# Kernel optimization log

Measured on AMD Instinct MI355X. Metric: run time of the kernel, lower is better.

The kernel has to match this reference:

```python
import jax, jax.numpy as jnp
import numpy as np

IN_DIM = 256
CODE_LEN = 128
MEM_LEN = 65536
BETA = 1.0


def setup_inputs() -> dict:
    key = jax.random.key(0)
    k1, k2, k3, k4, k5, k6 = jax.random.split(key, 6)
    x = jax.random.normal(k1, (1, IN_DIM), dtype=jnp.float32)
    memory = jax.random.normal(k2, (MEM_LEN, CODE_LEN), dtype=jnp.float32)
    mem_data = jax.random.normal(k3, (MEM_LEN, IN_DIM), dtype=jnp.float32)
    mem_idx = jnp.arange(MEM_LEN, dtype=jnp.int64) if jax.config.jax_enable_x64 else jnp.arange(MEM_LEN, dtype=jnp.int32)
    W = jax.random.normal(k4, (CODE_LEN, IN_DIM), dtype=jnp.float32) / np.sqrt(IN_DIM)
    b = jax.random.normal(k5, (CODE_LEN,), dtype=jnp.float32) * 0.01
    count = jnp.array(0, dtype=jnp.int32)
    return {"x": x, "memory": memory, "mem_data": mem_data, "mem_idx": mem_idx,
            "W": W, "b": b, "count": count}


def reference(x, memory, mem_data, mem_idx, W, b, count):
    # mean/std normalization using memory bank statistics (torch .std uses ddof=1)
    mean = mem_data.mean(axis=0)                      # [in_dim]
    std = mem_data.std(axis=0, ddof=1)                # [in_dim]
    new = (x - mean) / std
    new = jnp.where(std == 0, 0.0, new)               # [1, in_dim]
    # linear encode
    enc = new @ W.T + b                               # [1, code_len]
    # L1 distance to every memory slot, take min
    dists = jnp.sum(jnp.abs(memory - enc), axis=1)    # [mem_len]
    loss = dists.min()
    # conditional scatter update of memory / mem_data / mem_idx
    do_update = loss <= BETA
    pos = jnp.argmin(mem_idx)
    new_memory = jnp.where(do_update,
                           memory.at[pos].set(enc[0]), memory)
    new_mem_data = jnp.where(do_update,
                             mem_data.at[pos].set(x[0]), mem_data)
    new_mem_idx = jnp.where(do_update,
                            mem_idx.at[pos].set(count.astype(mem_idx.dtype)), mem_idx)
    return loss, new_memory, new_mem_data, new_mem_idx
```

## Files before the change

kernel.cpp:

```cpp
#include <hip/hip_runtime.h>
#include <hip/hip_bf16.h>

#define IN_DIM   256
#define CODE_LEN 128
#define MEM_LEN  65536
#define BETA     1.0f

#define OUT_MEM_OFF   1
#define OUT_MD_OFF    (1 + MEM_LEN*CODE_LEN)
#define OUT_IDX_OFF   (OUT_MD_OFF + MEM_LEN*IN_DIM)

#define WS_COLSUM 0
#define WS_COLSQ  256
#define WS_ENC    512
#define WS_LOSS   640
#define WS_KEY    642
#define WS_CTR2   644

#define MD_ELEMS  (MEM_LEN*IN_DIM)
#define MD_TILES  (MD_ELEMS/4)
#define MEM_ELEMS (MEM_LEN*CODE_LEN)
#define MEM_TILES (MEM_ELEMS/4)

typedef float vfloat4 __attribute__((ext_vector_type(4)));

__device__ __forceinline__ void store16u(float* dst, vfloat4 v) {
    __builtin_memcpy(dst, &v, 16);
}

__global__ void k_init(float* __restrict__ ws) {
    const int t = threadIdx.x;
    #pragma unroll
    for (int j = 0; j < 8; ++j) ws[t + j * 64] = 0.f;
    if (t == 0) {
        ((unsigned int*)ws)[WS_LOSS] = 0xFFFFFFFFu;
        *((unsigned long long*)(ws + WS_KEY)) = ~0ull;
        ((unsigned int*)ws)[WS_CTR2] = 0u;
    }
}

__global__ __launch_bounds__(256, 4) void k_stats_enc(
        const float* __restrict__ x,
        const float* __restrict__ mem_data,
        const int*   __restrict__ mem_idx,
        const float* __restrict__ W,
        const float* __restrict__ b,
        float* __restrict__ out,
        float* __restrict__ ws) {
    const int t = threadIdx.x;

    if (blockIdx.x >= 1024) {
        __shared__ unsigned long long red[256];
        const int tid = (blockIdx.x - 1024) * 256 + t;
        unsigned long long local = ~0ull;
        #pragma unroll
        for (int rep = 0; rep < 4; ++rep) {
            int i = tid + rep * 16384;
            int v = mem_idx[i];
            out[OUT_IDX_OFF + i] = (float)v;
            unsigned long long key =
                (((unsigned long long)(unsigned int)(v ^ (int)0x80000000)) << 32)
                | (unsigned int)i;
            local = local < key ? local : key;
        }
        red[t] = local;
        __syncthreads();
        for (int s = 128; s > 0; s >>= 1) {
            if (t < s) { unsigned long long o = red[t + s]; if (o < red[t]) red[t] = o; }
            __syncthreads();
        }
        if (t == 0) atomicMin((unsigned long long*)(ws + WS_KEY), red[0]);
    } else {
        __shared__ float lsum[256], lsq[256];
        float* __restrict__ out_md = out + OUT_MD_OFF;
        const int t0 = blockIdx.x * 256 + t;
        float s0=0,s1=0,s2=0,s3=0,q0=0,q1=0,q2=0,q3=0;

        vfloat4 v[16];
        #pragma unroll
        for (int j = 0; j < 16; ++j)
            v[j] = ((const vfloat4*)mem_data)[t0 + j * 262144];
        #pragma unroll
        for (int j = 0; j < 16; ++j) {
            const int k = t0 + j * 262144;
            store16u(out_md + 4 * k, v[j]);
            s0 += v[j].x; q0 += v[j].x * v[j].x;
            s1 += v[j].y; q1 += v[j].y * v[j].y;
            s2 += v[j].z; q2 += v[j].z * v[j].z;
            s3 += v[j].w; q3 += v[j].w * v[j].w;
        }

        lsum[t] = 0.f; lsq[t] = 0.f;
        __syncthreads();
        const int c0 = (4 * t) & 255;
        atomicAdd(&lsum[c0    ], s0);  atomicAdd(&lsq[c0    ], q0);
        atomicAdd(&lsum[c0 + 1], s1);  atomicAdd(&lsq[c0 + 1], q1);
        atomicAdd(&lsum[c0 + 2], s2);  atomicAdd(&lsq[c0 + 2], q2);
        atomicAdd(&lsum[c0 + 3], s3);  atomicAdd(&lsq[c0 + 3], q3);
        __syncthreads();
        atomicAdd(&ws[WS_COLSUM + t], lsum[t]);
        atomicAdd(&ws[WS_COLSQ  + t], lsq[t]);
    }

    asm volatile("s_waitcnt vmcnt(0)" ::: "memory");
    __syncthreads();
    __shared__ unsigned int s_last;
    if (t == 0)
        s_last = (atomicAdd(&((unsigned int*)ws)[WS_CTR2], 1u) == 1087u) ? 1u : 0u;
    __syncthreads();
    if (!s_last) return;

    __shared__ float nrm[IN_DIM];
    {
        float sum = atomicAdd(&ws[WS_COLSUM + t], 0.0f);
        float sq  = atomicAdd(&ws[WS_COLSQ  + t], 0.0f);
        float mean = sum * (1.0f / MEM_LEN);
        float var  = (sq - sum * sum * (1.0f / MEM_LEN)) * (1.0f / (MEM_LEN - 1));
        var = fmaxf(var, 0.0f);
        float sd = sqrtf(var);
        nrm[t] = (sd == 0.0f) ? 0.0f : (x[t] - mean) / sd;
    }
    __syncthreads();
    if (t < CODE_LEN) {
        float acc = b[t];
        const float* w = W + t * IN_DIM;
        #pragma unroll 8
        for (int d = 0; d < IN_DIM; ++d) acc += nrm[d] * w[d];
        ws[WS_ENC + t] = acc;
    }
}

__global__ __launch_bounds__(256, 4) void k_dist_copy(
        const float* __restrict__ memory,
        float* __restrict__ out,
        float* __restrict__ ws) {
    __shared__ vfloat4 es[32];
    __shared__ float red[256];
    const int t = threadIdx.x;
    if (t < 32) es[t] = ((const vfloat4*)(ws + WS_ENC))[t];
    __syncthreads();
    const int lane = t & 31;
    const int grp  = t >> 5;
    const vfloat4 e = es[lane];
    float* __restrict__ out_mem = out + OUT_MEM_OFF;
    float localmin = 3.4e38f;
    #pragma unroll
    for (int half = 0; half < 2; ++half) {
        vfloat4 m[4];
        int idx[4];
        #pragma unroll
        for (int sw = 0; sw < 4; ++sw) {
            const int row = (half * 4 + sw) * 8192 + blockIdx.x * 8 + grp;
            const int i = row * 32 + lane;
            idx[sw] = i;
            m[sw] = ((const vfloat4*)memory)[i];
        }
        #pragma unroll
        for (int sw = 0; sw < 4; ++sw) {
            const int i = idx[sw];
            store16u(out_mem + 4 * i, m[sw]);
            float d = fabsf(m[sw].x-e.x) + fabsf(m[sw].y-e.y)
                    + fabsf(m[sw].z-e.z) + fabsf(m[sw].w-e.w);
            #pragma unroll
            for (int off = 16; off > 0; off >>= 1) d += __shfl_xor(d, off, 32);
            localmin = fminf(localmin, d);
        }
    }
    red[t] = localmin;
    __syncthreads();
    for (int s2 = 128; s2 > 0; s2 >>= 1) {
        if (t < s2) red[t] = fminf(red[t], red[t + s2]);
        __syncthreads();
    }
    if (t == 0)
        atomicMin((unsigned int*)(ws + WS_LOSS), __float_as_uint(red[0]));
}

__global__ void k_final(const float* __restrict__ x,
                        const int* __restrict__ count,
                        const float* __restrict__ ws,
                        float* __restrict__ d_out) {
    const int t = threadIdx.x;
    const float loss = __uint_as_float(((const unsigned int*)ws)[WS_LOSS]);
    if (t == 0) d_out[0] = loss;
    if (loss <= BETA) {
        unsigned long long key = *(const unsigned long long*)(ws + WS_KEY);
        unsigned int pos = (unsigned int)(key & 0xFFFFFFFFull);
        if (t < CODE_LEN)
            d_out[OUT_MEM_OFF + (size_t)pos * CODE_LEN + t] = ws[WS_ENC + t];
        d_out[OUT_MD_OFF + (size_t)pos * IN_DIM + t] = x[t];
        if (t == 0)
            d_out[OUT_IDX_OFF + pos] = (float)count[0];
    }
}

extern "C" void kernel_launch(void* const* d_in, const int* in_sizes, int n_in,
                              void* d_out, int out_size, void* d_ws, size_t ws_size,
                              hipStream_t stream) {
    const float* x        = (const float*)d_in[0];
    const float* memory   = (const float*)d_in[1];
    const float* mem_data = (const float*)d_in[2];
    const int*   mem_idx  = (const int*)d_in[3];
    const float* W        = (const float*)d_in[4];
    const float* b        = (const float*)d_in[5];
    const int*   count    = (const int*)d_in[6];
    float* out = (float*)d_out;
    float* ws  = (float*)d_ws;

    k_init<<<1, 64, 0, stream>>>(ws);
    k_stats_enc<<<1088, 256, 0, stream>>>(x, mem_data, mem_idx, W, b, out, ws);
    k_dist_copy<<<1024, 256, 0, stream>>>(memory, out, ws);
    k_final<<<1, 256, 0, stream>>>(x, count, ws, out);
}
```

Before: 220.7 us.

## Split stats and encode kernels, widen grids, replicate atomic accumulators

Replaces the last-block-done counter with a separate single-block encode kernel. The column-stat atomics are spread over 16 replicated partial-sum slots, placed in the not-yet-written memory region of the output, and the loss atomicMin is spread over 8 slots. The stats and distance kernels now use 4x and 2x more blocks, each doing less work per thread, with a higher occupancy hint. The aim is less atomic contention, more memory-level parallelism and no serialized tail block, at the cost of one extra kernel launch and reuse of output memory as scratch.

```diff
diff --git a/kernel.cpp b/kernel.cpp
--- a/kernel.cpp
+++ b/kernel.cpp
@@ -1,5 +1,4 @@
 #include <hip/hip_runtime.h>
-#include <hip/hip_bf16.h>
 
 #define IN_DIM   256
 #define CODE_LEN 128
@@ -10,17 +9,15 @@
 #define OUT_MD_OFF    (1 + MEM_LEN*CODE_LEN)
 #define OUT_IDX_OFF   (OUT_MD_OFF + MEM_LEN*IN_DIM)
 
-#define WS_COLSUM 0
-#define WS_COLSQ  256
-#define WS_ENC    512
-#define WS_LOSS   640
-#define WS_KEY    642
-#define WS_CTR2   644
-
-#define MD_ELEMS  (MEM_LEN*IN_DIM)
-#define MD_TILES  (MD_ELEMS/4)
-#define MEM_ELEMS (MEM_LEN*CODE_LEN)
-#define MEM_TILES (MEM_ELEMS/4)
+#define WS_ENC   0
+#define WS_LOSS  128
+#define WS_KEY   136
+
+#define SB_OFF    OUT_MEM_OFF
+#define N_REP     16
+
+#define MD_TILES  (MEM_LEN*IN_DIM/4)
+#define MEM_TILES (MEM_LEN*CODE_LEN/4)
 
 typedef float vfloat4 __attribute__((ext_vector_type(4)));
 
@@ -28,30 +25,25 @@
     __builtin_memcpy(dst, &v, 16);
 }
 
-__global__ void k_init(float* __restrict__ ws) {
-    const int t = threadIdx.x;
-    #pragma unroll
-    for (int j = 0; j < 8; ++j) ws[t + j * 64] = 0.f;
-    if (t == 0) {
-        ((unsigned int*)ws)[WS_LOSS] = 0xFFFFFFFFu;
-        *((unsigned long long*)(ws + WS_KEY)) = ~0ull;
-        ((unsigned int*)ws)[WS_CTR2] = 0u;
-    }
-}
-
-__global__ __launch_bounds__(256, 4) void k_stats_enc(
-        const float* __restrict__ x,
+__global__ void k_init(float* __restrict__ out, float* __restrict__ ws) {
+    const int t = threadIdx.x;
+    #pragma unroll
+    for (int j = 0; j < 2 * N_REP; ++j) out[SB_OFF + t + j * 256] = 0.f;
+    if (t < 8) ((unsigned int*)ws)[WS_LOSS + t] = 0xFFFFFFFFu;
+    if (t == 0) *((unsigned long long*)(ws + WS_KEY)) = ~0ull;
+}
+
+__global__ __launch_bounds__(256, 8) void k_stats(
         const float* __restrict__ mem_data,
         const int*   __restrict__ mem_idx,
-        const float* __restrict__ W,
-        const float* __restrict__ b,
         float* __restrict__ out,
         float* __restrict__ ws) {
     const int t = threadIdx.x;
-
-    if (blockIdx.x >= 1024) {
+    const int bid = blockIdx.x;
+
+    if (bid >= 4096) {
         __shared__ unsigned long long red[256];
-        const int tid = (blockIdx.x - 1024) * 256 + t;
+        const int tid = (bid - 4096) * 256 + t;
         unsigned long long local = ~0ull;
         #pragma unroll
         for (int rep = 0; rep < 4; ++rep) {
@@ -70,56 +62,59 @@
             __syncthreads();
         }
         if (t == 0) atomicMin((unsigned long long*)(ws + WS_KEY), red[0]);
-    } else {
-        __shared__ float lsum[256], lsq[256];
-        float* __restrict__ out_md = out + OUT_MD_OFF;
-        const int t0 = blockIdx.x * 256 + t;
-        float s0=0,s1=0,s2=0,s3=0,q0=0,q1=0,q2=0,q3=0;
-
-        vfloat4 v[16];
-        #pragma unroll
-        for (int j = 0; j < 16; ++j)
-            v[j] = ((const vfloat4*)mem_data)[t0 + j * 262144];
-        #pragma unroll
-        for (int j = 0; j < 16; ++j) {
-            const int k = t0 + j * 262144;
-            store16u(out_md + 4 * k, v[j]);
-            s0 += v[j].x; q0 += v[j].x * v[j].x;
-            s1 += v[j].y; q1 += v[j].y * v[j].y;
-            s2 += v[j].z; q2 += v[j].z * v[j].z;
-            s3 += v[j].w; q3 += v[j].w * v[j].w;
-        }
-
-        lsum[t] = 0.f; lsq[t] = 0.f;
-        __syncthreads();
-        const int c0 = (4 * t) & 255;
-        atomicAdd(&lsum[c0    ], s0);  atomicAdd(&lsq[c0    ], q0);
-        atomicAdd(&lsum[c0 + 1], s1);  atomicAdd(&lsq[c0 + 1], q1);
-        atomicAdd(&lsum[c0 + 2], s2);  atomicAdd(&lsq[c0 + 2], q2);
-        atomicAdd(&lsum[c0 + 3], s3);  atomicAdd(&lsq[c0 + 3], q3);
-        __syncthreads();
-        atomicAdd(&ws[WS_COLSUM + t], lsum[t]);
-        atomicAdd(&ws[WS_COLSQ  + t], lsq[t]);
-    }
-
-    asm volatile("s_waitcnt vmcnt(0)" ::: "memory");
-    __syncthreads();
-    __shared__ unsigned int s_last;
-    if (t == 0)
-        s_last = (atomicAdd(&((unsigned int*)ws)[WS_CTR2], 1u) == 1087u) ? 1u : 0u;
-    __syncthreads();
-    if (!s_last) return;
-
+        return;
+    }
+
+    __shared__ float lsum[256], lsq[256];
+    lsum[t] = 0.f; lsq[t] = 0.f;
+    __syncthreads();
+
+    float* __restrict__ out_md = out + OUT_MD_OFF;
+    const int gtid = bid * 256 + t;
+    float s0=0,s1=0,s2=0,s3=0,q0=0,q1=0,q2=0,q3=0;
+
+    vfloat4 v[4];
+    #pragma unroll
+    for (int i = 0; i < 4; ++i)
+        v[i] = ((const vfloat4*)mem_data)[gtid + i * 1048576];
+    #pragma unroll
+    for (int i = 0; i < 4; ++i) {
+        store16u(out_md + 4 * (gtid + i * 1048576), v[i]);
+        s0 += v[i].x; q0 += v[i].x * v[i].x;
+        s1 += v[i].y; q1 += v[i].y * v[i].y;
+        s2 += v[i].z; q2 += v[i].z * v[i].z;
+        s3 += v[i].w; q3 += v[i].w * v[i].w;
+    }
+
+    const int c0 = (4 * t) & 255;
+    atomicAdd(&lsum[c0    ], s0);  atomicAdd(&lsq[c0    ], q0);
+    atomicAdd(&lsum[c0 + 1], s1);  atomicAdd(&lsq[c0 + 1], q1);
+    atomicAdd(&lsum[c0 + 2], s2);  atomicAdd(&lsq[c0 + 2], q2);
+    atomicAdd(&lsum[c0 + 3], s3);  atomicAdd(&lsq[c0 + 3], q3);
+    __syncthreads();
+    float* __restrict__ sb = out + SB_OFF + (bid & (N_REP - 1)) * 512;
+    atomicAdd(&sb[t      ], lsum[t]);
+    atomicAdd(&sb[t + 256], lsq[t]);
+}
+
+__global__ void k_enc(const float* __restrict__ x,
+                      const float* __restrict__ W,
+                      const float* __restrict__ b,
+                      const float* __restrict__ out,
+                      float* __restrict__ ws) {
     __shared__ float nrm[IN_DIM];
-    {
-        float sum = atomicAdd(&ws[WS_COLSUM + t], 0.0f);
-        float sq  = atomicAdd(&ws[WS_COLSQ  + t], 0.0f);
-        float mean = sum * (1.0f / MEM_LEN);
-        float var  = (sq - sum * sum * (1.0f / MEM_LEN)) * (1.0f / (MEM_LEN - 1));
-        var = fmaxf(var, 0.0f);
-        float sd = sqrtf(var);
-        nrm[t] = (sd == 0.0f) ? 0.0f : (x[t] - mean) / sd;
-    }
+    const int t = threadIdx.x;
+    float sum = 0.f, sq = 0.f;
+    #pragma unroll
+    for (int r = 0; r < N_REP; ++r) {
+        sum += out[SB_OFF + r * 512 + t];
+        sq  += out[SB_OFF + r * 512 + 256 + t];
+    }
+    float mean = sum * (1.0f / MEM_LEN);
+    float var  = (sq - sum * sum * (1.0f / MEM_LEN)) * (1.0f / (MEM_LEN - 1));
+    var = fmaxf(var, 0.0f);
+    float sd = sqrtf(var);
+    nrm[t] = (sd == 0.0f) ? 0.0f : (x[t] - mean) / sd;
     __syncthreads();
     if (t < CODE_LEN) {
         float acc = b[t];
@@ -130,7 +125,7 @@
     }
 }
 
-__global__ __launch_bounds__(256, 4) void k_dist_copy(
+__global__ __launch_bounds__(256, 8) void k_dist(
         const float* __restrict__ memory,
         float* __restrict__ out,
         float* __restrict__ ws) {
@@ -140,32 +135,25 @@
     if (t < 32) es[t] = ((const vfloat4*)(ws + WS_ENC))[t];
     __syncthreads();
     const int lane = t & 31;
-    const int grp  = t >> 5;
     const vfloat4 e = es[lane];
     float* __restrict__ out_mem = out + OUT_MEM_OFF;
+    const int gtid = blockIdx.x * 256 + t;
     float localmin = 3.4e38f;
-    #pragma unroll
-    for (int half = 0; half < 2; ++half) {
-        vfloat4 m[4];
-        int idx[4];
+
+    vfloat4 m[4];
+    #pragma unroll
+    for (int i = 0; i < 4; ++i)
+        m[i] = ((const vfloat4*)memory)[gtid + i * 524288];
+    #pragma unroll
+    for (int i = 0; i < 4; ++i) {
+        store16u(out_mem + 4 * (gtid + i * 524288), m[i]);
+        float d = fabsf(m[i].x - e.x) + fabsf(m[i].y - e.y)
+                + fabsf(m[i].z - e.z) + fabsf(m[i].w - e.w);
         #pragma unroll
-        for (int sw = 0; sw < 4; ++sw) {
-            const int row = (half * 4 + sw) * 8192 + blockIdx.x * 8 + grp;
-            const int i = row * 32 + lane;
-            idx[sw] = i;
-            m[sw] = ((const vfloat4*)memory)[i];
-        }
-        #pragma unroll
-        for (int sw = 0; sw < 4; ++sw) {
-            const int i = idx[sw];
-            store16u(out_mem + 4 * i, m[sw]);
-            float d = fabsf(m[sw].x-e.x) + fabsf(m[sw].y-e.y)
-                    + fabsf(m[sw].z-e.z) + fabsf(m[sw].w-e.w);
-            #pragma unroll
-            for (int off = 16; off > 0; off >>= 1) d += __shfl_xor(d, off, 32);
-            localmin = fminf(localmin, d);
-        }
-    }
+        for (int off = 16; off > 0; off >>= 1) d += __shfl_xor(d, off, 32);
+        localmin = fminf(localmin, d);
+    }
+
     red[t] = localmin;
     __syncthreads();
     for (int s2 = 128; s2 > 0; s2 >>= 1) {
@@ -173,7 +161,8 @@
         __syncthreads();
     }
     if (t == 0)
-        atomicMin((unsigned int*)(ws + WS_LOSS), __float_as_uint(red[0]));
+        atomicMin((unsigned int*)(ws + WS_LOSS + (blockIdx.x & 7)),
+                  __float_as_uint(red[0]));
 }
 
 __global__ void k_final(const float* __restrict__ x,
@@ -181,7 +170,13 @@
                         const float* __restrict__ ws,
                         float* __restrict__ d_out) {
     const int t = threadIdx.x;
-    const float loss = __uint_as_float(((const unsigned int*)ws)[WS_LOSS]);
+    unsigned int lb = ((const unsigned int*)ws)[WS_LOSS];
+    #pragma unroll
+    for (int r = 1; r < 8; ++r) {
+        unsigned int o = ((const unsigned int*)ws)[WS_LOSS + r];
+        lb = o < lb ? o : lb;
+    }
+    const float loss = __uint_as_float(lb);
     if (t == 0) d_out[0] = loss;
     if (loss <= BETA) {
         unsigned long long key = *(const unsigned long long*)(ws + WS_KEY);
@@ -207,8 +202,9 @@
     float* out = (float*)d_out;
     float* ws  = (float*)d_ws;
 
-    k_init<<<1, 64, 0, stream>>>(ws);
-    k_stats_enc<<<1088, 256, 0, stream>>>(x, mem_data, mem_idx, W, b, out, ws);
-    k_dist_copy<<<1024, 256, 0, stream>>>(memory, out, ws);
+    k_init<<<1, 256, 0, stream>>>(out, ws);
+    k_stats<<<4160, 256, 0, stream>>>(mem_data, mem_idx, out, ws);
+    k_enc<<<1, 256, 0, stream>>>(x, W, b, out, ws);
+    k_dist<<<2048, 256, 0, stream>>>(memory, out, ws);
     k_final<<<1, 256, 0, stream>>>(x, count, ws, out);
 }
```

Result: slower. 239.0 us (+8.3%).

## Offload output copies to hipMemcpyAsync and split encode into separate kernel

Applied to the files above, without the earlier changes.

Moves the bulk copy of mem_data and memory into the output buffers out of the fused compute kernels and into device-to-device async memcpys. The stats and distance kernels become read-only, and the last-block-done encode step becomes a standalone single-block kernel. This is meant to simplify the kernels and raise occupancy via launch bounds. In exchange, the input arrays are now read twice, once by the copy and once by the compute kernels, which adds global memory traffic.

```diff
diff --git a/kernel.cpp b/kernel.cpp
--- a/kernel.cpp
+++ b/kernel.cpp
@@ -1,5 +1,4 @@
 #include <hip/hip_runtime.h>
-#include <hip/hip_bf16.h>
 
 #define IN_DIM   256
 #define CODE_LEN 128
@@ -15,18 +14,11 @@
 #define WS_ENC    512
 #define WS_LOSS   640
 #define WS_KEY    642
-#define WS_CTR2   644
 
 #define MD_ELEMS  (MEM_LEN*IN_DIM)
-#define MD_TILES  (MD_ELEMS/4)
 #define MEM_ELEMS (MEM_LEN*CODE_LEN)
-#define MEM_TILES (MEM_ELEMS/4)
 
 typedef float vfloat4 __attribute__((ext_vector_type(4)));
-
-__device__ __forceinline__ void store16u(float* dst, vfloat4 v) {
-    __builtin_memcpy(dst, &v, 16);
-}
 
 __global__ void k_init(float* __restrict__ ws) {
     const int t = threadIdx.x;
@@ -35,23 +27,20 @@
     if (t == 0) {
         ((unsigned int*)ws)[WS_LOSS] = 0xFFFFFFFFu;
         *((unsigned long long*)(ws + WS_KEY)) = ~0ull;
-        ((unsigned int*)ws)[WS_CTR2] = 0u;
     }
 }
 
-__global__ __launch_bounds__(256, 4) void k_stats_enc(
-        const float* __restrict__ x,
+__global__ __launch_bounds__(256, 8) void k_stats_read(
         const float* __restrict__ mem_data,
         const int*   __restrict__ mem_idx,
-        const float* __restrict__ W,
-        const float* __restrict__ b,
         float* __restrict__ out,
         float* __restrict__ ws) {
     const int t = threadIdx.x;
+    const int bid = blockIdx.x;
 
-    if (blockIdx.x >= 1024) {
+    if (bid >= 1024) {
         __shared__ unsigned long long red[256];
-        const int tid = (blockIdx.x - 1024) * 256 + t;
+        const int tid = (bid - 1024) * 256 + t;
         unsigned long long local = ~0ull;
         #pragma unroll
         for (int rep = 0; rep < 4; ++rep) {
@@ -70,56 +59,51 @@
             __syncthreads();
         }
         if (t == 0) atomicMin((unsigned long long*)(ws + WS_KEY), red[0]);
-    } else {
-        __shared__ float lsum[256], lsq[256];
-        float* __restrict__ out_md = out + OUT_MD_OFF;
-        const int t0 = blockIdx.x * 256 + t;
-        float s0=0,s1=0,s2=0,s3=0,q0=0,q1=0,q2=0,q3=0;
-
-        vfloat4 v[16];
-        #pragma unroll
-        for (int j = 0; j < 16; ++j)
-            v[j] = ((const vfloat4*)mem_data)[t0 + j * 262144];
-        #pragma unroll
-        for (int j = 0; j < 16; ++j) {
-            const int k = t0 + j * 262144;
-            store16u(out_md + 4 * k, v[j]);
-            s0 += v[j].x; q0 += v[j].x * v[j].x;
-            s1 += v[j].y; q1 += v[j].y * v[j].y;
-            s2 += v[j].z; q2 += v[j].z * v[j].z;
-            s3 += v[j].w; q3 += v[j].w * v[j].w;
-        }
-
-        lsum[t] = 0.f; lsq[t] = 0.f;
-        __syncthreads();
-        const int c0 = (4 * t) & 255;
-        atomicAdd(&lsum[c0    ], s0);  atomicAdd(&lsq[c0    ], q0);
-        atomicAdd(&lsum[c0 + 1], s1);  atomicAdd(&lsq[c0 + 1], q1);
-        atomicAdd(&lsum[c0 + 2], s2);  atomicAdd(&lsq[c0 + 2], q2);
-        atomicAdd(&lsum[c0 + 3], s3);  atomicAdd(&lsq[c0 + 3], q3);
-        __syncthreads();
-        atomicAdd(&ws[WS_COLSUM + t], lsum[t]);
-        atomicAdd(&ws[WS_COLSQ  + t], lsq[t]);
+        return;
     }
 
-    asm volatile("s_waitcnt vmcnt(0)" ::: "memory");
+    __shared__ float lsum[256], lsq[256];
+    lsum[t] = 0.f; lsq[t] = 0.f;
+
+    const int gtid = bid * 256 + t;
+    float s0=0,s1=0,s2=0,s3=0,q0=0,q1=0,q2=0,q3=0;
+
+    vfloat4 v[16];
+    #pragma unroll
+    for (int j = 0; j < 16; ++j)
+        v[j] = ((const vfloat4*)mem_data)[gtid + j * 262144];
+    #pragma unroll
+    for (int j = 0; j < 16; ++j) {
+        s0 += v[j].x; q0 += v[j].x * v[j].x;
+        s1 += v[j].y; q1 += v[j].y * v[j].y;
+        s2 += v[j].z; q2 += v[j].z * v[j].z;
+        s3 += v[j].w; q3 += v[j].w * v[j].w;
+    }
+
     __syncthreads();
-    __shared__ unsigned int s_last;
-    if (t == 0)
-        s_last = (atomicAdd(&((unsigned int*)ws)[WS_CTR2], 1u) == 1087u) ? 1u : 0u;
+    const int c0 = (4 * t) & 255;
+    atomicAdd(&lsum[c0    ], s0);  atomicAdd(&lsq[c0    ], q0);
+    atomicAdd(&lsum[c0 + 1], s1);  atomicAdd(&lsq[c0 + 1], q1);
+    atomicAdd(&lsum[c0 + 2], s2);  atomicAdd(&lsq[c0 + 2], q2);
+    atomicAdd(&lsum[c0 + 3], s3);  atomicAdd(&lsq[c0 + 3], q3);
     __syncthreads();
-    if (!s_last) return;
+    atomicAdd(&ws[WS_COLSUM + t], lsum[t]);
+    atomicAdd(&ws[WS_COLSQ  + t], lsq[t]);
+}
 
+__global__ void k_enc(const float* __restrict__ x,
+                      const float* __restrict__ W,
+                      const float* __restrict__ b,
+                      float* __restrict__ ws) {
     __shared__ float nrm[IN_DIM];
-    {
-        float sum = atomicAdd(&ws[WS_COLSUM + t], 0.0f);
-        float sq  = atomicAdd(&ws[WS_COLSQ  + t], 0.0f);
-        float mean = sum * (1.0f / MEM_LEN);
-        float var  = (sq - sum * sum * (1.0f / MEM_LEN)) * (1.0f / (MEM_LEN - 1));
-        var = fmaxf(var, 0.0f);
-        float sd = sqrtf(var);
-        nrm[t] = (sd == 0.0f) ? 0.0f : (x[t] - mean) / sd;
-    }
+    const int t = threadIdx.x;
+    float sum = ws[WS_COLSUM + t];
+    float sq  = ws[WS_COLSQ + t];
+    float mean = sum * (1.0f / MEM_LEN);
+    float var  = (sq - sum * sum * (1.0f / MEM_LEN)) * (1.0f / (MEM_LEN - 1));
+    var = fmaxf(var, 0.0f);
+    float sd = sqrtf(var);
+    nrm[t] = (sd == 0.0f) ? 0.0f : (x[t] - mean) / sd;
     __syncthreads();
     if (t < CODE_LEN) {
         float acc = b[t];
@@ -130,9 +114,8 @@
     }
 }
 
-__global__ __launch_bounds__(256, 4) void k_dist_copy(
+__global__ __launch_bounds__(256, 8) void k_dist_read(
         const float* __restrict__ memory,
-        float* __restrict__ out,
         float* __restrict__ ws) {
     __shared__ vfloat4 es[32];
     __shared__ float red[256];
@@ -142,30 +125,23 @@
     const int lane = t & 31;
     const int grp  = t >> 5;
     const vfloat4 e = es[lane];
-    float* __restrict__ out_mem = out + OUT_MEM_OFF;
     float localmin = 3.4e38f;
+
+    vfloat4 m[8];
     #pragma unroll
-    for (int half = 0; half < 2; ++half) {
-        vfloat4 m[4];
-        int idx[4];
+    for (int i = 0; i < 8; ++i) {
+        const int row = i * 8192 + blockIdx.x * 8 + grp;
+        m[i] = ((const vfloat4*)memory)[row * 32 + lane];
+    }
+    #pragma unroll
+    for (int i = 0; i < 8; ++i) {
+        float d = fabsf(m[i].x - e.x) + fabsf(m[i].y - e.y)
+                + fabsf(m[i].z - e.z) + fabsf(m[i].w - e.w);
         #pragma unroll
-        for (int sw = 0; sw < 4; ++sw) {
-            const int row = (half * 4 + sw) * 8192 + blockIdx.x * 8 + grp;
-            const int i = row * 32 + lane;
-            idx[sw] = i;
-            m[sw] = ((const vfloat4*)memory)[i];
-        }
-        #pragma unroll
-        for (int sw = 0; sw < 4; ++sw) {
-            const int i = idx[sw];
-            store16u(out_mem + 4 * i, m[sw]);
-            float d = fabsf(m[sw].x-e.x) + fabsf(m[sw].y-e.y)
-                    + fabsf(m[sw].z-e.z) + fabsf(m[sw].w-e.w);
-            #pragma unroll
-            for (int off = 16; off > 0; off >>= 1) d += __shfl_xor(d, off, 32);
-            localmin = fminf(localmin, d);
-        }
+        for (int off = 16; off > 0; off >>= 1) d += __shfl_xor(d, off, 32);
+        localmin = fminf(localmin, d);
     }
+
     red[t] = localmin;
     __syncthreads();
     for (int s2 = 128; s2 > 0; s2 >>= 1) {
@@ -208,7 +184,14 @@
     float* ws  = (float*)d_ws;
 
     k_init<<<1, 64, 0, stream>>>(ws);
-    k_stats_enc<<<1088, 256, 0, stream>>>(x, mem_data, mem_idx, W, b, out, ws);
-    k_dist_copy<<<1024, 256, 0, stream>>>(memory, out, ws);
+
+    hipMemcpyAsync(out + OUT_MD_OFF,  mem_data, (size_t)MD_ELEMS  * 4,
+                   hipMemcpyDeviceToDevice, stream);
+    hipMemcpyAsync(out + OUT_MEM_OFF, memory,   (size_t)MEM_ELEMS * 4,
+                   hipMemcpyDeviceToDevice, stream);
+
+    k_stats_read<<<1088, 256, 0, stream>>>(mem_data, mem_idx, out, ws);
+    k_enc<<<1, 256, 0, stream>>>(x, W, b, ws);
+    k_dist_read<<<1024, 256, 0, stream>>>(memory, ws);
     k_final<<<1, 256, 0, stream>>>(x, count, ws, out);
 }
```

New measurement: 282.6 us. 28.0% more time.
